# Kernel optimization log

Hardware: AMD Instinct MI355X
Metric: run time of the kernel (lower is better)

Reference implementation:

```python
import jax, jax.numpy as jnp
import numpy as np

EPS = 1e-3  # matches module default eps=0.001


def setup_inputs() -> dict:
    key = jax.random.key(0)
    k1, k2 = jax.random.split(key)
    B, C, W, H = 8, 64, 496, 432  # KITTI BEV grid, pillar feature dim 64
    x = jax.random.normal(k1, (B, C, W, H), dtype=jnp.float32)
    # are exactly zero across all channels so x.sum(1) == 0 there.
    occ = (jax.random.uniform(k2, (B, W, H)) < 0.10).astype(jnp.float32)
    x = x * occ[:, None, :, :]
    return {"x": x}


def reference(x):
    # Faithful to the torch module, including its padding artifact: each batch's
    # nonzero index list is padded to N = max(num_nonzeros) with index (0,0), so
    # padded slots gather x[b,:,0,0], contribute to mean/var with multiplicity
    # (N - n_b), and scatter a normalized value back into pixel (0,0).
    B, C, Wd, Hd = x.shape
    mask = (x.sum(axis=1) != 0)                 # [B,W,H] occupied pixels
    n = mask.sum(axis=(1, 2))                    # [B] nonzeros per batch
    N = n.max()                                  # padded gather length
    pad = (N - n).astype(x.dtype)                # [B] number of (0,0) pad slots
    x00 = x[:, :, 0, 0]                          # [B,C] value gathered by pads
    mb = mask[:, None, :, :].astype(x.dtype)     # [B,1,W,H]

    count = (B * N).astype(x.dtype)              # total gathered entries
    total = (x * mb).sum(axis=(0, 2, 3)) + (pad[:, None] * x00).sum(axis=0)  # [C]
    mean = total / count                         # [C]

    d = x - mean[None, :, None, None]
    sq = ((d * d) * mb).sum(axis=(0, 2, 3)) + (pad[:, None] * (x00 - mean) ** 2).sum(axis=0)
    var = sq / count                             # [C] biased variance (mean over gathered)

    inv = 1.0 / jnp.sqrt(var + EPS)              # [C]; note: mean is NOT subtracted
    out = jnp.where(mask[:, None, :, :], x * inv[None, :, None, None], x)

    # scatter-back hits (0,0) whenever batch b had pad slots OR (0,0) was nonzero
    write00 = (pad > 0) | mask[:, 0, 0]          # [B]
    out = out.at[:, :, 0, 0].set(
        jnp.where(write00[:, None], x00 * inv[None, :], out[:, :, 0, 0])
    )
    return out
```

## Files before the change

### kernel.cpp

```cpp
#include <hip/hip_runtime.h>

#define WH      214272
#define GPB     53568
#define TOTAL4  (512*GPB)
#define CHUNKS  (TOTAL4/64)
#define CPP     (GPB/64)

#define STATS_BLOCKS 1024
#define NWAVES (STATS_BLOCKS*4)
#define PER ((CHUNKS + NWAVES - 1)/NWAVES)

#define SCALE_BLOCKS 2048

#define NREP   16
#define WS_FLOATS (NREP*64*2 + 64)

typedef float floatx4 __attribute__((ext_vector_type(4)));

__global__ __launch_bounds__(256, 4) void k_stats(const floatx4* __restrict__ x4,
                                                  float* __restrict__ gsum,
                                                  float* __restrict__ gsq,
                                                  int* __restrict__ gn) {
    const int lane = threadIdx.x & 63;
    const int gw   = blockIdx.x * 4 + (threadIdx.x >> 6);
    const int rep  = gw & (NREP - 1);
    int c0 = gw * PER;
    const int c1 = min(c0 + PER, CHUNKS);

    while (c0 < c1) {
        const int plane = (int)((unsigned)c0 / CPP);
        const int run   = min(c1, (plane + 1) * CPP);
        const bool isC0 = (plane & 63) == 0;

        float s0 = 0.f, s1 = 0.f, s2 = 0.f, s3 = 0.f;
        float q0 = 0.f, q1 = 0.f, q2 = 0.f, q3 = 0.f;
        int cnt = 0;
        const floatx4* p = x4 + (size_t)c0 * 64 + lane;
        const int n = run - c0;
        int k = 0;
        for (; k + 8 <= n; k += 8) {
            const floatx4 v0 = p[(size_t)(k + 0) * 64];
            const floatx4 v1 = p[(size_t)(k + 1) * 64];
            const floatx4 v2 = p[(size_t)(k + 2) * 64];
            const floatx4 v3 = p[(size_t)(k + 3) * 64];
            const floatx4 v4 = p[(size_t)(k + 4) * 64];
            const floatx4 v5 = p[(size_t)(k + 5) * 64];
            const floatx4 v6 = p[(size_t)(k + 6) * 64];
            const floatx4 v7 = p[(size_t)(k + 7) * 64];
            s0 += (v0.x + v0.y) + (v0.z + v0.w);
            s1 += (v1.x + v1.y) + (v1.z + v1.w);
            s2 += (v2.x + v2.y) + (v2.z + v2.w);
            s3 += (v3.x + v3.y) + (v3.z + v3.w);
            q0 = fmaf(v0.w, v0.w, fmaf(v0.z, v0.z, fmaf(v0.y, v0.y, fmaf(v0.x, v0.x, q0))));
            q1 = fmaf(v1.w, v1.w, fmaf(v1.z, v1.z, fmaf(v1.y, v1.y, fmaf(v1.x, v1.x, q1))));
            q2 = fmaf(v2.w, v2.w, fmaf(v2.z, v2.z, fmaf(v2.y, v2.y, fmaf(v2.x, v2.x, q2))));
            q3 = fmaf(v3.w, v3.w, fmaf(v3.z, v3.z, fmaf(v3.y, v3.y, fmaf(v3.x, v3.x, q3))));
            s0 += (v4.x + v4.y) + (v4.z + v4.w);
            s1 += (v5.x + v5.y) + (v5.z + v5.w);
            s2 += (v6.x + v6.y) + (v6.z + v6.w);
            s3 += (v7.x + v7.y) + (v7.z + v7.w);
            q0 = fmaf(v4.w, v4.w, fmaf(v4.z, v4.z, fmaf(v4.y, v4.y, fmaf(v4.x, v4.x, q0))));
            q1 = fmaf(v5.w, v5.w, fmaf(v5.z, v5.z, fmaf(v5.y, v5.y, fmaf(v5.x, v5.x, q1))));
            q2 = fmaf(v6.w, v6.w, fmaf(v6.z, v6.z, fmaf(v6.y, v6.y, fmaf(v6.x, v6.x, q2))));
            q3 = fmaf(v7.w, v7.w, fmaf(v7.z, v7.z, fmaf(v7.y, v7.y, fmaf(v7.x, v7.x, q3))));
            if (isC0) {
                cnt += (v0.x != 0.f) + (v0.y != 0.f) + (v0.z != 0.f) + (v0.w != 0.f);
                cnt += (v1.x != 0.f) + (v1.y != 0.f) + (v1.z != 0.f) + (v1.w != 0.f);
                cnt += (v2.x != 0.f) + (v2.y != 0.f) + (v2.z != 0.f) + (v2.w != 0.f);
                cnt += (v3.x != 0.f) + (v3.y != 0.f) + (v3.z != 0.f) + (v3.w != 0.f);
                cnt += (v4.x != 0.f) + (v4.y != 0.f) + (v4.z != 0.f) + (v4.w != 0.f);
                cnt += (v5.x != 0.f) + (v5.y != 0.f) + (v5.z != 0.f) + (v5.w != 0.f);
                cnt += (v6.x != 0.f) + (v6.y != 0.f) + (v6.z != 0.f) + (v6.w != 0.f);
                cnt += (v7.x != 0.f) + (v7.y != 0.f) + (v7.z != 0.f) + (v7.w != 0.f);
            }
        }
        for (; k < n; ++k) {
            const floatx4 v = p[(size_t)k * 64];
            s0 += (v.x + v.y) + (v.z + v.w);
            q0 = fmaf(v.w, v.w, fmaf(v.z, v.z, fmaf(v.y, v.y, fmaf(v.x, v.x, q0))));
            if (isC0) cnt += (v.x != 0.f) + (v.y != 0.f) + (v.z != 0.f) + (v.w != 0.f);
        }
        float s = (s0 + s1) + (s2 + s3);
        float q = (q0 + q1) + (q2 + q3);
#pragma unroll
        for (int m = 1; m < 64; m <<= 1) {
            s += __shfl_xor(s, m, 64);
            q += __shfl_xor(q, m, 64);
        }
        if (isC0) {
#pragma unroll
            for (int m = 1; m < 64; m <<= 1) cnt += __shfl_xor(cnt, m, 64);
        }
        if (lane == 0) {
            atomicAdd(&gsum[rep * 64 + (plane & 63)], s);
            atomicAdd(&gsq[rep * 64 + (plane & 63)], q);
            if (isC0) atomicAdd(&gn[(rep & 7) * 8 + (plane >> 6)], cnt);
        }
        c0 = run;
    }
}

__global__ __launch_bounds__(256, 8) void k_scale(const floatx4* __restrict__ x4,
                                                  floatx4* __restrict__ out4,
                                                  const float* __restrict__ gsum,
                                                  const float* __restrict__ gsq,
                                                  const int* __restrict__ gn) {
    __shared__ float sinv[64];
    const int tid = threadIdx.x;
    if (tid < 64) {
        const int c = tid;
        const float* x = (const float*)x4;
        float total = 0.f, S2 = 0.f;
#pragma unroll
        for (int r = 0; r < NREP; ++r) {
            total += gsum[r * 64 + c];
            S2    += gsq[r * 64 + c];
        }
        int nb[8];
        int N = 0;
#pragma unroll
        for (int b = 0; b < 8; ++b) {
            int v = 0;
#pragma unroll
            for (int r = 0; r < 8; ++r) v += gn[r * 8 + b];
            nb[b] = v;
            N = max(N, v);
        }
#pragma unroll
        for (int b = 0; b < 8; ++b) {
            const float pad = (float)(N - nb[b]);
            const float x00 = x[(size_t)(b * 64 + c) * WH];
            total = fmaf(pad, x00, total);
            S2    = fmaf(pad, x00 * x00, S2);
        }
        const float count = (float)(8 * N);
        const float mean  = total / count;
        const float var   = S2 / count - mean * mean;
        sinv[c] = 1.0f / sqrtf(var + 0.001f);
    }
    __syncthreads();

    const int lane = tid & 63;
    const int gw   = blockIdx.x * 4 + (tid >> 6);
    const int run  = gw >> 1;
    const int sub  = gw & 1;
    const int c0   = run * PER;
    const int c1   = min(c0 + PER, CHUNKS);
#pragma unroll 4
    for (int ch = c1 - 1 - sub; ch >= c0; ch -= 2) {
        const int plane = (int)((unsigned)ch / CPP);
        const float inv = sinv[plane & 63];
        const size_t i = (size_t)ch * 64 + lane;
        floatx4 v = __builtin_nontemporal_load(&x4[i]);
        v.x *= inv; v.y *= inv; v.z *= inv; v.w *= inv;
        __builtin_nontemporal_store(v, &out4[i]);
    }
}

extern "C" void kernel_launch(void* const* d_in, const int* in_sizes, int n_in,
                              void* d_out, int out_size, void* d_ws, size_t ws_size,
                              hipStream_t stream) {
    const float* x  = (const float*)d_in[0];
    float* out      = (float*)d_out;
    float* wsf      = (float*)d_ws;
    float* gsum     = wsf;
    float* gsq      = wsf + NREP * 64;
    int*   gn       = (int*)(wsf + NREP * 128);

    (void)hipMemsetAsync(d_ws, 0, WS_FLOATS * sizeof(float), stream);

    k_stats<<<STATS_BLOCKS, 256, 0, stream>>>((const floatx4*)x, gsum, gsq, gn);
    k_scale<<<SCALE_BLOCKS, 256, 0, stream>>>((const floatx4*)x, (floatx4*)out,
                                              gsum, gsq, gn);
}
```

Baseline: 765.3 us.

## Align stats and scale sweeps so scale pass reuses cache-resident data

The stats kernel now uses the same per-wave chunk partition as the scale kernel and walks its range backward. It reads the first NTCH chunks of each range with nontemporal loads and the rest with normal loads. The scale kernel drops the two-wave interleave and walks each range backward from the end, so the most recently read data, still likely in L2/MALL, is consumed first. Stats occupancy rises to 8 blocks per CU with 2048 blocks. The added complexity risks tail imbalance, and the cache reuse depends on the caches being large enough.

```diff
diff --git a/kernel.cpp b/kernel.cpp
--- a/kernel.cpp
+++ b/kernel.cpp
@@ -6,97 +6,119 @@
 #define CHUNKS  (TOTAL4/64)
 #define CPP     (GPB/64)
 
-#define STATS_BLOCKS 1024
-#define NWAVES (STATS_BLOCKS*4)
-#define PER ((CHUNKS + NWAVES - 1)/NWAVES)
+#define BLOCKS  2048
+#define NW      (BLOCKS*4)
+#define PER     ((CHUNKS + NW - 1)/NW)
+#define NTCH    25
 
-#define SCALE_BLOCKS 2048
-
-#define NREP   16
+#define NREP    16
 #define WS_FLOATS (NREP*64*2 + 64)
 
 typedef float floatx4 __attribute__((ext_vector_type(4)));
 
-__global__ __launch_bounds__(256, 4) void k_stats(const floatx4* __restrict__ x4,
+template<bool NT>
+__device__ __forceinline__ void sweep(const floatx4* __restrict__ base, int lo, int hi,
+                                      float& s0, float& s1, float& s2, float& s3,
+                                      float& q0, float& q1, float& q2, float& q3,
+                                      int& cnt, const bool isC0) {
+    int k = hi;
+    while (k - 6 >= lo) {
+        k -= 6;
+        floatx4 v0, v1, v2, v3, v4, v5;
+        if (NT) {
+            v0 = __builtin_nontemporal_load(&base[(size_t)(k + 5) * 64]);
+            v1 = __builtin_nontemporal_load(&base[(size_t)(k + 4) * 64]);
+            v2 = __builtin_nontemporal_load(&base[(size_t)(k + 3) * 64]);
+            v3 = __builtin_nontemporal_load(&base[(size_t)(k + 2) * 64]);
+            v4 = __builtin_nontemporal_load(&base[(size_t)(k + 1) * 64]);
+            v5 = __builtin_nontemporal_load(&base[(size_t)(k + 0) * 64]);
+        } else {
+            v0 = base[(size_t)(k + 5) * 64];
+            v1 = base[(size_t)(k + 4) * 64];
+            v2 = base[(size_t)(k + 3) * 64];
+            v3 = base[(size_t)(k + 2) * 64];
+            v4 = base[(size_t)(k + 1) * 64];
+            v5 = base[(size_t)(k + 0) * 64];
+        }
+        s0 += (v0.x + v0.y) + (v0.z + v0.w);
+        s1 += (v1.x + v1.y) + (v1.z + v1.w);
+        s2 += (v2.x + v2.y) + (v2.z + v2.w);
+        s3 += (v3.x + v3.y) + (v3.z + v3.w);
+        q0 = fmaf(v0.w, v0.w, fmaf(v0.z, v0.z, fmaf(v0.y, v0.y, fmaf(v0.x, v0.x, q0))));
+        q1 = fmaf(v1.w, v1.w, fmaf(v1.z, v1.z, fmaf(v1.y, v1.y, fmaf(v1.x, v1.x, q1))));
+        q2 = fmaf(v2.w, v2.w, fmaf(v2.z, v2.z, fmaf(v2.y, v2.y, fmaf(v2.x, v2.x, q2))));
+        q3 = fmaf(v3.w, v3.w, fmaf(v3.z, v3.z, fmaf(v3.y, v3.y, fmaf(v3.x, v3.x, q3))));
+        s0 += (v4.x + v4.y) + (v4.z + v4.w);
+        s1 += (v5.x + v5.y) + (v5.z + v5.w);
+        q0 = fmaf(v4.w, v4.w, fmaf(v4.z, v4.z, fmaf(v4.y, v4.y, fmaf(v4.x, v4.x, q0))));
+        q1 = fmaf(v5.w, v5.w, fmaf(v5.z, v5.z, fmaf(v5.y, v5.y, fmaf(v5.x, v5.x, q1))));
+        if (isC0) {
+            cnt += (v0.x != 0.f) + (v0.y != 0.f) + (v0.z != 0.f) + (v0.w != 0.f);
+            cnt += (v1.x != 0.f) + (v1.y != 0.f) + (v1.z != 0.f) + (v1.w != 0.f);
+            cnt += (v2.x != 0.f) + (v2.y != 0.f) + (v2.z != 0.f) + (v2.w != 0.f);
+            cnt += (v3.x != 0.f) + (v3.y != 0.f) + (v3.z != 0.f) + (v3.w != 0.f);
+            cnt += (v4.x != 0.f) + (v4.y != 0.f) + (v4.z != 0.f) + (v4.w != 0.f);
+            cnt += (v5.x != 0.f) + (v5.y != 0.f) + (v5.z != 0.f) + (v5.w != 0.f);
+        }
+    }
+    while (k > lo) {
+        --k;
+        floatx4 v;
+        if (NT) v = __builtin_nontemporal_load(&base[(size_t)k * 64]);
+        else    v = base[(size_t)k * 64];
+        s0 += (v.x + v.y) + (v.z + v.w);
+        q0 = fmaf(v.w, v.w, fmaf(v.z, v.z, fmaf(v.y, v.y, fmaf(v.x, v.x, q0))));
+        if (isC0) cnt += (v.x != 0.f) + (v.y != 0.f) + (v.z != 0.f) + (v.w != 0.f);
+    }
+}
+
+__global__ __launch_bounds__(256, 8) void k_stats(const floatx4* __restrict__ x4,
                                                   float* __restrict__ gsum,
                                                   float* __restrict__ gsq,
                                                   int* __restrict__ gn) {
     const int lane = threadIdx.x & 63;
     const int gw   = blockIdx.x * 4 + (threadIdx.x >> 6);
     const int rep  = gw & (NREP - 1);
-    int c0 = gw * PER;
-    const int c1 = min(c0 + PER, CHUNKS);
+    const int c0   = gw * PER;
+    const int c1   = min(c0 + PER, CHUNKS);
+    if (c0 >= c1) return;
+    const int split = c0 + NTCH;
+    const floatx4* base = x4 + lane;
 
-    while (c0 < c1) {
-        const int plane = (int)((unsigned)c0 / CPP);
-        const int run   = min(c1, (plane + 1) * CPP);
+    int e = c1;
+    while (e > c0) {
+        const int plane = (int)((unsigned)(e - 1) / CPP);
+        const int s = max(c0, plane * CPP);
         const bool isC0 = (plane & 63) == 0;
 
         float s0 = 0.f, s1 = 0.f, s2 = 0.f, s3 = 0.f;
         float q0 = 0.f, q1 = 0.f, q2 = 0.f, q3 = 0.f;
         int cnt = 0;
-        const floatx4* p = x4 + (size_t)c0 * 64 + lane;
-        const int n = run - c0;
-        int k = 0;
-        for (; k + 8 <= n; k += 8) {
-            const floatx4 v0 = p[(size_t)(k + 0) * 64];
-            const floatx4 v1 = p[(size_t)(k + 1) * 64];
-            const floatx4 v2 = p[(size_t)(k + 2) * 64];
-            const floatx4 v3 = p[(size_t)(k + 3) * 64];
-            const floatx4 v4 = p[(size_t)(k + 4) * 64];
-            const floatx4 v5 = p[(size_t)(k + 5) * 64];
-            const floatx4 v6 = p[(size_t)(k + 6) * 64];
-            const floatx4 v7 = p[(size_t)(k + 7) * 64];
-            s0 += (v0.x + v0.y) + (v0.z + v0.w);
-            s1 += (v1.x + v1.y) + (v1.z + v1.w);
-            s2 += (v2.x + v2.y) + (v2.z + v2.w);
-            s3 += (v3.x + v3.y) + (v3.z + v3.w);
-            q0 = fmaf(v0.w, v0.w, fmaf(v0.z, v0.z, fmaf(v0.y, v0.y, fmaf(v0.x, v0.x, q0))));
-            q1 = fmaf(v1.w, v1.w, fmaf(v1.z, v1.z, fmaf(v1.y, v1.y, fmaf(v1.x, v1.x, q1))));
-            q2 = fmaf(v2.w, v2.w, fmaf(v2.z, v2.z, fmaf(v2.y, v2.y, fmaf(v2.x, v2.x, q2))));
-            q3 = fmaf(v3.w, v3.w, fmaf(v3.z, v3.z, fmaf(v3.y, v3.y, fmaf(v3.x, v3.x, q3))));
-            s0 += (v4.x + v4.y) + (v4.z + v4.w);
-            s1 += (v5.x + v5.y) + (v5.z + v5.w);
-            s2 += (v6.x + v6.y) + (v6.z + v6.w);
-            s3 += (v7.x + v7.y) + (v7.z + v7.w);
-            q0 = fmaf(v4.w, v4.w, fmaf(v4.z, v4.z, fmaf(v4.y, v4.y, fmaf(v4.x, v4.x, q0))));
-            q1 = fmaf(v5.w, v5.w, fmaf(v5.z, v5.z, fmaf(v5.y, v5.y, fmaf(v5.x, v5.x, q1))));
-            q2 = fmaf(v6.w, v6.w, fmaf(v6.z, v6.z, fmaf(v6.y, v6.y, fmaf(v6.x, v6.x, q2))));
-            q3 = fmaf(v7.w, v7.w, fmaf(v7.z, v7.z, fmaf(v7.y, v7.y, fmaf(v7.x, v7.x, q3))));
-            if (isC0) {
-                cnt += (v0.x != 0.f) + (v0.y != 0.f) + (v0.z != 0.f) + (v0.w != 0.f);
-                cnt += (v1.x != 0.f) + (v1.y != 0.f) + (v1.z != 0.f) + (v1.w != 0.f);
-                cnt += (v2.x != 0.f) + (v2.y != 0.f) + (v2.z != 0.f) + (v2.w != 0.f);
-                cnt += (v3.x != 0.f) + (v3.y != 0.f) + (v3.z != 0.f) + (v3.w != 0.f);
-                cnt += (v4.x != 0.f) + (v4.y != 0.f) + (v4.z != 0.f) + (v4.w != 0.f);
-                cnt += (v5.x != 0.f) + (v5.y != 0.f) + (v5.z != 0.f) + (v5.w != 0.f);
-                cnt += (v6.x != 0.f) + (v6.y != 0.f) + (v6.z != 0.f) + (v6.w != 0.f);
-                cnt += (v7.x != 0.f) + (v7.y != 0.f) + (v7.z != 0.f) + (v7.w != 0.f);
-            }
-        }
-        for (; k < n; ++k) {
-            const floatx4 v = p[(size_t)k * 64];
-            s0 += (v.x + v.y) + (v.z + v.w);
-            q0 = fmaf(v.w, v.w, fmaf(v.z, v.z, fmaf(v.y, v.y, fmaf(v.x, v.x, q0))));
-            if (isC0) cnt += (v.x != 0.f) + (v.y != 0.f) + (v.z != 0.f) + (v.w != 0.f);
-        }
-        float s = (s0 + s1) + (s2 + s3);
-        float q = (q0 + q1) + (q2 + q3);
+
+        const int pl = max(s, split);
+        if (e > pl)
+            sweep<false>(base, pl, e, s0, s1, s2, s3, q0, q1, q2, q3, cnt, isC0);
+        const int nthi = min(e, split);
+        if (nthi > s)
+            sweep<true>(base, s, nthi, s0, s1, s2, s3, q0, q1, q2, q3, cnt, isC0);
+
+        float ss = (s0 + s1) + (s2 + s3);
+        float qq = (q0 + q1) + (q2 + q3);
 #pragma unroll
         for (int m = 1; m < 64; m <<= 1) {
-            s += __shfl_xor(s, m, 64);
-            q += __shfl_xor(q, m, 64);
+            ss += __shfl_xor(ss, m, 64);
+            qq += __shfl_xor(qq, m, 64);
         }
         if (isC0) {
 #pragma unroll
             for (int m = 1; m < 64; m <<= 1) cnt += __shfl_xor(cnt, m, 64);
         }
         if (lane == 0) {
-            atomicAdd(&gsum[rep * 64 + (plane & 63)], s);
-            atomicAdd(&gsq[rep * 64 + (plane & 63)], q);
+            atomicAdd(&gsum[rep * 64 + (plane & 63)], ss);
+            atomicAdd(&gsq[rep * 64 + (plane & 63)], qq);
             if (isC0) atomicAdd(&gn[(rep & 7) * 8 + (plane >> 6)], cnt);
         }
-        c0 = run;
+        e = s;
     }
 }
 
@@ -142,12 +164,10 @@
 
     const int lane = tid & 63;
     const int gw   = blockIdx.x * 4 + (tid >> 6);
-    const int run  = gw >> 1;
-    const int sub  = gw & 1;
-    const int c0   = run * PER;
+    const int c0   = gw * PER;
     const int c1   = min(c0 + PER, CHUNKS);
 #pragma unroll 4
-    for (int ch = c1 - 1 - sub; ch >= c0; ch -= 2) {
+    for (int ch = c1 - 1; ch >= c0; --ch) {
         const int plane = (int)((unsigned)ch / CPP);
         const float inv = sinv[plane & 63];
         const size_t i = (size_t)ch * 64 + lane;
@@ -169,7 +189,7 @@
 
     (void)hipMemsetAsync(d_ws, 0, WS_FLOATS * sizeof(float), stream);
 
-    k_stats<<<STATS_BLOCKS, 256, 0, stream>>>((const floatx4*)x, gsum, gsq, gn);
-    k_scale<<<SCALE_BLOCKS, 256, 0, stream>>>((const floatx4*)x, (floatx4*)out,
-                                              gsum, gsq, gn);
+    k_stats<<<BLOCKS, 256, 0, stream>>>((const floatx4*)x, gsum, gsq, gn);
+    k_scale<<<BLOCKS, 256, 0, stream>>>((const floatx4*)x, (floatx4*)out,
+                                        gsum, gsq, gn);
 }
```

Result: no change. 760.9 us (-0.6%).

## Split stats and scale passes into halves to reuse last-level cache

Applied to the files above, without the earlier changes.

Both the stats and scale kernels now take a base offset and process half of the tensor per launch. Stats runs first half then second half, and scale runs second half first, so recently read data may still be resident in the large last-level cache. Scale loads are changed from nontemporal to regular loads to allow cache hits. This adds two extra kernel launches, and the benefit depends on a half-tensor (~220MB) fitting in the cache.

```diff
diff --git a/kernel.cpp b/kernel.cpp
--- a/kernel.cpp
+++ b/kernel.cpp
@@ -5,14 +5,13 @@
 #define TOTAL4  (512*GPB)
 #define CHUNKS  (TOTAL4/64)
 #define CPP     (GPB/64)
+#define HALF_CH (CHUNKS/2)
 
-#define STATS_BLOCKS 1024
-#define NWAVES (STATS_BLOCKS*4)
-#define PER ((CHUNKS + NWAVES - 1)/NWAVES)
+#define SBLK    1024
+#define SW      (SBLK*4)
+#define SPER    ((HALF_CH + SW - 1)/SW)
 
-#define SCALE_BLOCKS 2048
-
-#define NREP   16
+#define NREP    16
 #define WS_FLOATS (NREP*64*2 + 64)
 
 typedef float floatx4 __attribute__((ext_vector_type(4)));
@@ -20,12 +19,13 @@
 __global__ __launch_bounds__(256, 4) void k_stats(const floatx4* __restrict__ x4,
                                                   float* __restrict__ gsum,
                                                   float* __restrict__ gsq,
-                                                  int* __restrict__ gn) {
+                                                  int* __restrict__ gn,
+                                                  int base) {
     const int lane = threadIdx.x & 63;
     const int gw   = blockIdx.x * 4 + (threadIdx.x >> 6);
     const int rep  = gw & (NREP - 1);
-    int c0 = gw * PER;
-    const int c1 = min(c0 + PER, CHUNKS);
+    int c0 = base + gw * SPER;
+    const int c1 = min(c0 + SPER, base + HALF_CH);
 
     while (c0 < c1) {
         const int plane = (int)((unsigned)c0 / CPP);
@@ -80,20 +80,20 @@
             q0 = fmaf(v.w, v.w, fmaf(v.z, v.z, fmaf(v.y, v.y, fmaf(v.x, v.x, q0))));
             if (isC0) cnt += (v.x != 0.f) + (v.y != 0.f) + (v.z != 0.f) + (v.w != 0.f);
         }
-        float s = (s0 + s1) + (s2 + s3);
-        float q = (q0 + q1) + (q2 + q3);
+        float ss = (s0 + s1) + (s2 + s3);
+        float qq = (q0 + q1) + (q2 + q3);
 #pragma unroll
         for (int m = 1; m < 64; m <<= 1) {
-            s += __shfl_xor(s, m, 64);
-            q += __shfl_xor(q, m, 64);
+            ss += __shfl_xor(ss, m, 64);
+            qq += __shfl_xor(qq, m, 64);
         }
         if (isC0) {
 #pragma unroll
             for (int m = 1; m < 64; m <<= 1) cnt += __shfl_xor(cnt, m, 64);
         }
         if (lane == 0) {
-            atomicAdd(&gsum[rep * 64 + (plane & 63)], s);
-            atomicAdd(&gsq[rep * 64 + (plane & 63)], q);
+            atomicAdd(&gsum[rep * 64 + (plane & 63)], ss);
+            atomicAdd(&gsq[rep * 64 + (plane & 63)], qq);
             if (isC0) atomicAdd(&gn[(rep & 7) * 8 + (plane >> 6)], cnt);
         }
         c0 = run;
@@ -104,7 +104,8 @@
                                                   floatx4* __restrict__ out4,
                                                   const float* __restrict__ gsum,
                                                   const float* __restrict__ gsq,
-                                                  const int* __restrict__ gn) {
+                                                  const int* __restrict__ gn,
+                                                  int base) {
     __shared__ float sinv[64];
     const int tid = threadIdx.x;
     if (tid < 64) {
@@ -142,16 +143,14 @@
 
     const int lane = tid & 63;
     const int gw   = blockIdx.x * 4 + (tid >> 6);
-    const int run  = gw >> 1;
-    const int sub  = gw & 1;
-    const int c0   = run * PER;
-    const int c1   = min(c0 + PER, CHUNKS);
+    const int c0   = base + gw * SPER;
+    const int c1   = min(c0 + SPER, base + HALF_CH);
 #pragma unroll 4
-    for (int ch = c1 - 1 - sub; ch >= c0; ch -= 2) {
+    for (int ch = c1 - 1; ch >= c0; --ch) {
         const int plane = (int)((unsigned)ch / CPP);
         const float inv = sinv[plane & 63];
         const size_t i = (size_t)ch * 64 + lane;
-        floatx4 v = __builtin_nontemporal_load(&x4[i]);
+        floatx4 v = x4[i];
         v.x *= inv; v.y *= inv; v.z *= inv; v.w *= inv;
         __builtin_nontemporal_store(v, &out4[i]);
     }
@@ -169,7 +168,10 @@
 
     (void)hipMemsetAsync(d_ws, 0, WS_FLOATS * sizeof(float), stream);
 
-    k_stats<<<STATS_BLOCKS, 256, 0, stream>>>((const floatx4*)x, gsum, gsq, gn);
-    k_scale<<<SCALE_BLOCKS, 256, 0, stream>>>((const floatx4*)x, (floatx4*)out,
-                                              gsum, gsq, gn);
+    k_stats<<<SBLK, 256, 0, stream>>>((const floatx4*)x, gsum, gsq, gn, 0);
+    k_stats<<<SBLK, 256, 0, stream>>>((const floatx4*)x, gsum, gsq, gn, HALF_CH);
+    k_scale<<<SBLK, 256, 0, stream>>>((const floatx4*)x, (floatx4*)out,
+                                      gsum, gsq, gn, HALF_CH);
+    k_scale<<<SBLK, 256, 0, stream>>>((const floatx4*)x, (floatx4*)out,
+                                      gsum, gsq, gn, 0);
 }
```

Result: slower. 784.4 us (+2.5%).
